# Kernel tuning notes

Measured on AMD Instinct MI355X. Metric: run time of the kernel, lower is better.

## Reference

```python
import jax, jax.numpy as jnp
import numpy as np

N_NODES = 102400
N_EDGES = 1638400
DIMS = [128, 64, 32, 1]  # decoder_dim=128, decoder_l=3, last layer -> 1


def setup_inputs() -> dict:
    key = jax.random.key(0)
    ks = jax.random.split(key, 10)
    inp = {
        'b_z': jax.random.normal(ks[0], (N_NODES, DIMS[0]), jnp.float32),
        'src': jax.random.randint(ks[1], (N_EDGES,), 0, N_NODES, jnp.int64 if jax.config.jax_enable_x64 else jnp.int32),
        'dst': jax.random.randint(ks[2], (N_EDGES,), 0, N_NODES, jnp.int64 if jax.config.jax_enable_x64 else jnp.int32),
        'edge_weight': jax.random.uniform(ks[3], (N_EDGES,), jnp.float32),
        'b_size': 100,
    }
    # GraphConv weights: W [in, out], bias [out] (DGL xavier init; randn ok for ref)
    for i in range(3):
        inp[f'W{i}'] = jax.random.normal(ks[4 + i], (DIMS[i], DIMS[i + 1]), jnp.float32) * (1.0 / np.sqrt(DIMS[i]))
        inp[f'b{i}'] = jnp.zeros((DIMS[i + 1],), jnp.float32)
    return inp


def _gcn_layer(h, src, dst, ew, W, b, activate):
    n = h.shape[0]
    ones = jnp.ones((src.shape[0],), h.dtype)
    # norm='both': symmetric degree normalization with plain (unweighted) degrees
    out_deg = jnp.clip(jax.ops.segment_sum(ones, src, num_segments=n), 1.0)
    in_deg = jnp.clip(jax.ops.segment_sum(ones, dst, num_segments=n), 1.0)
    h = h * (out_deg ** -0.5)[:, None]
    h = h @ W  # in_feats > out_feats: transform before aggregation (DGL order)
    msg = h[src] * ew[:, None]           # [E, out] edge-weighted gather
    agg = jax.ops.segment_sum(msg, dst, num_segments=n)  # scatter-add
    agg = agg * (in_deg ** -0.5)[:, None] + b
    return jnp.tanh(agg) if activate else agg


def reference(b_z, src, dst, edge_weight, b_size, W0, b0, W1, b1, W2, b2):
    h = b_z
    h = _gcn_layer(h, src, dst, edge_weight, W0, b0, True)
    h = _gcn_layer(h, src, dst, edge_weight, W1, b1, True)
    h = _gcn_layer(h, src, dst, edge_weight, W2, b2, False)
    return h.reshape(b_size, -1)
```

## Files before the change

kernel.cpp:

```cpp
#include <hip/hip_runtime.h>
#include <hip/hip_fp16.h>
#include <math.h>

#define N_NODES 102400
#define N_EDGES 1638400
#define NB 100
#define PB 256
#define EPB (N_EDGES/PB)

union H4 { int2 i2; __half h[4]; };

__global__ __launch_bounds__(256) void histA_kernel(const int* __restrict__ src, const int* __restrict__ dst,
                                                    int* __restrict__ histD, int* __restrict__ histS) {
    __shared__ int hD[NB], hS[NB];
    int tid = threadIdx.x;
    if (tid < NB) { hD[tid] = 0; hS[tid] = 0; }
    __syncthreads();
    int base = blockIdx.x * EPB;
    for (int i = tid; i < EPB; i += 256) {
        atomicAdd(&hD[dst[base + i] >> 10], 1);
        atomicAdd(&hS[src[base + i] >> 10], 1);
    }
    __syncthreads();
    if (tid < NB) {
        histD[blockIdx.x * NB + tid] = hD[tid];
        histS[blockIdx.x * NB + tid] = hS[tid];
    }
}

__global__ __launch_bounds__(256) void scanB_kernel(const int* __restrict__ histD, const int* __restrict__ histS,
                                                    int* __restrict__ offD, int* __restrict__ offS,
                                                    int* __restrict__ coarseD, int* __restrict__ coarseS) {
    __shared__ int totD[NB], totS[NB], baseD[NB + 1], baseS[NB + 1];
    int t = threadIdx.x;
    if (t < NB) { int s = 0; for (int k = 0; k < PB; k++) s += histD[k * NB + t]; totD[t] = s; }
    else if (t >= 128 && t < 128 + NB) { int j = t - 128; int s = 0; for (int k = 0; k < PB; k++) s += histS[k * NB + j]; totS[j] = s; }
    __syncthreads();
    if (t == 0)   { int r = 0; for (int j = 0; j < NB; j++) { baseD[j] = r; r += totD[j]; } baseD[NB] = r; }
    if (t == 128) { int r = 0; for (int j = 0; j < NB; j++) { baseS[j] = r; r += totS[j]; } baseS[NB] = r; }
    __syncthreads();
    if (t < NB) { int r = baseD[t]; for (int k = 0; k < PB; k++) { offD[k * NB + t] = r; r += histD[k * NB + t]; } }
    else if (t >= 128 && t < 128 + NB) { int j = t - 128; int r = baseS[j]; for (int k = 0; k < PB; k++) { offS[k * NB + j] = r; r += histS[k * NB + j]; } }
    if (t <= NB) coarseD[t] = baseD[t];
    if (t >= 128 && t <= 128 + NB) coarseS[t - 128] = baseS[t - 128];
}

__global__ __launch_bounds__(256) void partC_kernel(const int* __restrict__ src, const int* __restrict__ dst,
                                                    const float* __restrict__ ew,
                                                    const int* __restrict__ offD, const int* __restrict__ offS,
                                                    int2* __restrict__ partD, int* __restrict__ partS) {
    __shared__ int cD[NB], cS[NB];
    int tid = threadIdx.x;
    if (tid < NB) { cD[tid] = offD[blockIdx.x * NB + tid]; cS[tid] = offS[blockIdx.x * NB + tid]; }
    __syncthreads();
    int base = blockIdx.x * EPB;
    for (int i = tid; i < EPB; i += 256) {
        int s = src[base + i], d = dst[base + i];
        float w = ew[base + i];
        int p = atomicAdd(&cD[d >> 10], 1);
        partD[p] = make_int2(s | ((d & 1023) << 17), __float_as_int(w));
        int q = atomicAdd(&cS[s >> 10], 1);
        partS[q] = s & 1023;
    }
}

__global__ __launch_bounds__(1024) void fineS_kernel(const int* __restrict__ partS, const int* __restrict__ coarseS,
                                                     float* __restrict__ outdeg_inv) {
    __shared__ int hist[1024];
    int tid = threadIdx.x;
    hist[tid] = 0;
    __syncthreads();
    int beg = coarseS[blockIdx.x], end = coarseS[blockIdx.x + 1];
    for (int i = beg + tid; i < end; i += 1024) atomicAdd(&hist[partS[i]], 1);
    __syncthreads();
    outdeg_inv[blockIdx.x * 1024 + tid] = 1.0f / sqrtf((float)max(hist[tid], 1));
}

__global__ __launch_bounds__(1024) void fineD_kernel(const int2* __restrict__ partD, const int* __restrict__ coarseD,
                                                     const float* __restrict__ outdeg_inv,
                                                     int2* __restrict__ edge_perm, int* __restrict__ row_off,
                                                     float* __restrict__ indeg_inv) {
    __shared__ int hist[1024], cursor[1024];
    __shared__ int wsum[16];
    int tid = threadIdx.x, lane = tid & 63, wid = tid >> 6;
    hist[tid] = 0;
    __syncthreads();
    int beg = coarseD[blockIdx.x], end = coarseD[blockIdx.x + 1];
    for (int i = beg + tid; i < end; i += 1024) atomicAdd(&hist[(partD[i].x >> 17) & 1023], 1);
    __syncthreads();
    int v = hist[tid];
    int x = v;
    #pragma unroll
    for (int s = 1; s < 64; s <<= 1) { int t = __shfl_up(x, s, 64); if (lane >= s) x += t; }
    if (lane == 63) wsum[wid] = x;
    __syncthreads();
    if (wid == 0) {
        int ws = (lane < 16) ? wsum[lane] : 0;
        int y = ws;
        #pragma unroll
        for (int s = 1; s < 16; s <<= 1) { int t = __shfl_up(y, s, 64); if (lane >= s) y += t; }
        if (lane < 16) wsum[lane] = y - ws;
    }
    __syncthreads();
    int ex = wsum[wid] + x - v;
    cursor[tid] = beg + ex;
    int node = blockIdx.x * 1024 + tid;
    row_off[node] = beg + ex;
    indeg_inv[node] = 1.0f / sqrtf((float)max(v, 1));
    if (blockIdx.x == NB - 1 && tid == 0) row_off[N_NODES] = N_EDGES;
    __syncthreads();
    for (int i = beg + tid; i < end; i += 1024) {
        int2 t2 = partD[i];
        int d = (t2.x >> 17) & 1023, s = t2.x & 0x1FFFF;
        int p = atomicAdd(&cursor[d], 1);
        float w = __int_as_float(t2.y) * outdeg_inv[s];
        edge_perm[p] = make_int2(s, __float_as_int(w));
    }
}

template<int K, int C, int RN>
__global__ __launch_bounds__(256) void gemm_tile_kernel(
    const float* __restrict__ h, const float* __restrict__ W, __half* __restrict__ out) {
    constexpr int BM = 64;
    constexpr int RM = 4;
    constexpr int KC = 64;
    constexpr int TX = C / RN;
    constexpr int TY = BM / RM;
    static_assert(TX * TY == 256, "bad tile");
    static_assert(RN == 4, "fp16 epilogue assumes RN==4");

    __shared__ float Ws[K * C];
    __shared__ float Hs[KC][BM + 4];

    const int tid = threadIdx.x;
    const long brow = (long)blockIdx.x * BM;

    for (int i = tid; i < K * C; i += 256) Ws[i] = W[i];

    const int tx = tid % TX;
    const int ty = tid / TX;
    float acc[RM][RN] = {};

    const int lr = tid % 16;
    const int lk = tid / 16;

    for (int kc = 0; kc < K; kc += KC) {
        __syncthreads();
        #pragma unroll
        for (int p0 = 0; p0 < BM; p0 += 16) {
            const int r = p0 + lr;
            const float4 hv = *(const float4*)(h + (brow + r) * K + kc + lk * 4);
            Hs[lk * 4 + 0][r] = hv.x;
            Hs[lk * 4 + 1][r] = hv.y;
            Hs[lk * 4 + 2][r] = hv.z;
            Hs[lk * 4 + 3][r] = hv.w;
        }
        __syncthreads();

        #pragma unroll
        for (int k = 0; k < KC; ++k) {
            const float4 a4 = *(const float4*)&Hs[k][ty * RM];
            const float av[RM] = {a4.x, a4.y, a4.z, a4.w};
            float b[RN];
            *(float4*)b = *(const float4*)&Ws[(kc + k) * C + tx * RN];
            #pragma unroll
            for (int i = 0; i < RM; ++i)
                #pragma unroll
                for (int j = 0; j < RN; ++j)
                    acc[i][j] += av[i] * b[j];
        }
    }

    #pragma unroll
    for (int i = 0; i < RM; ++i) {
        const long row = brow + ty * RM + i;
        __half2 p01 = __floats2half2_rn(acc[i][0], acc[i][1]);
        __half2 p23 = __floats2half2_rn(acc[i][2], acc[i][3]);
        int2 packed = make_int2(*(int*)&p01, *(int*)&p23);
        *(int2*)(out + row * C + tx * RN) = packed;
    }
}

__global__ __launch_bounds__(256) void agg64_gemm_kernel(
    const __half* __restrict__ ht, const int* __restrict__ row_off,
    const int2* __restrict__ ep, const float* __restrict__ indeg_inv,
    const float* __restrict__ b0, const float* __restrict__ W1,
    __half* __restrict__ ht1, int N) {
    __shared__ float W1s[64 * 32];
    __shared__ float h1s[4][64];
    int tid = threadIdx.x;
    {
        const float4* W1v = (const float4*)W1;
        float4* W1sv = (float4*)W1s;
        W1sv[tid] = W1v[tid];
        W1sv[tid + 256] = W1v[tid + 256];
    }
    __syncthreads();

    int wave = (blockIdx.x * blockDim.x + tid) >> 6;
    int lane = tid & 63;
    if (wave >= N) return;
    int chunk = lane & 15;
    int eslot = lane >> 4;
    int beg = row_off[wave], end = row_off[wave + 1];
    const char* htb = (const char*)ht;
    unsigned coff = (unsigned)(chunk << 3);

    float4 a0 = {0, 0, 0, 0}, a1 = {0, 0, 0, 0};
    for (int e = beg; e < end; e += 8) {
        int ei0 = e + eslot, ei1 = e + 4 + eslot;
        int2 d0 = ep[min(ei0, end - 1)];
        int2 d1 = ep[min(ei1, end - 1)];
        float w0 = (ei0 < end) ? __int_as_float(d0.y) : 0.0f;
        float w1 = (ei1 < end) ? __int_as_float(d1.y) : 0.0f;
        H4 r0, r1;
        r0.i2 = *(const int2*)(htb + (((unsigned)d0.x << 7) | coff));
        r1.i2 = *(const int2*)(htb + (((unsigned)d1.x << 7) | coff));
        a0.x = fmaf(__half2float(r0.h[0]), w0, a0.x);
        a0.y = fmaf(__half2float(r0.h[1]), w0, a0.y);
        a0.z = fmaf(__half2float(r0.h[2]), w0, a0.z);
        a0.w = fmaf(__half2float(r0.h[3]), w0, a0.w);
        a1.x = fmaf(__half2float(r1.h[0]), w1, a1.x);
        a1.y = fmaf(__half2float(r1.h[1]), w1, a1.y);
        a1.z = fmaf(__half2float(r1.h[2]), w1, a1.z);
        a1.w = fmaf(__half2float(r1.h[3]), w1, a1.w);
    }
    a0.x += a1.x; a0.y += a1.y; a0.z += a1.z; a0.w += a1.w;
    #pragma unroll
    for (int s = 16; s <= 32; s <<= 1) {
        a0.x += __shfl_xor(a0.x, s, 64);
        a0.y += __shfl_xor(a0.y, s, 64);
        a0.z += __shfl_xor(a0.z, s, 64);
        a0.w += __shfl_xor(a0.w, s, 64);
    }
    int wv = tid >> 6;
    if (eslot == 0) {
        float sc = indeg_inv[wave];
        float4 b = *(const float4*)(b0 + chunk * 4);
        float4 v;
        v.x = tanhf(a0.x * sc + b.x);
        v.y = tanhf(a0.y * sc + b.y);
        v.z = tanhf(a0.z * sc + b.z);
        v.w = tanhf(a0.w * sc + b.w);
        *(float4*)&h1s[wv][chunk * 4] = v;
    }
    int c = lane & 31, half = lane >> 5;
    float t = 0.0f;
    #pragma unroll
    for (int j4 = 0; j4 < 8; ++j4) {
        int k = half * 32 + j4 * 4;
        float4 hh = *(const float4*)&h1s[wv][k];
        t += hh.x * W1s[(k + 0) * 32 + c];
        t += hh.y * W1s[(k + 1) * 32 + c];
        t += hh.z * W1s[(k + 2) * 32 + c];
        t += hh.w * W1s[(k + 3) * 32 + c];
    }
    t += __shfl_xor(t, 32, 64);
    if (half == 0) ht1[(long)wave * 32 + c] = __float2half_rn(t);
}

__global__ void agg32_dot_kernel(const __half* __restrict__ ht, const int* __restrict__ row_off,
                                 const int2* __restrict__ ep,
                                 const float* __restrict__ indeg_inv, const float* __restrict__ bias,
                                 const float* __restrict__ W2, float* __restrict__ ht2, int N) {
    int wave = (blockIdx.x * blockDim.x + threadIdx.x) >> 6;
    int lane = threadIdx.x & 63;
    if (wave >= N) return;
    int chunk = lane & 7;
    int eslot = lane >> 3;
    int beg = row_off[wave], end = row_off[wave + 1];
    const char* htb = (const char*)ht;
    unsigned coff = (unsigned)(chunk << 3);
    float4 a0 = {0, 0, 0, 0}, a1 = {0, 0, 0, 0};
    for (int e = beg; e < end; e += 16) {
        int ei0 = e + eslot, ei1 = e + 8 + eslot;
        int2 d0 = ep[min(ei0, end - 1)];
        int2 d1 = ep[min(ei1, end - 1)];
        float w0 = (ei0 < end) ? __int_as_float(d0.y) : 0.0f;
        float w1 = (ei1 < end) ? __int_as_float(d1.y) : 0.0f;
        H4 r0, r1;
        r0.i2 = *(const int2*)(htb + (((unsigned)d0.x << 6) | coff));
        r1.i2 = *(const int2*)(htb + (((unsigned)d1.x << 6) | coff));
        a0.x = fmaf(__half2float(r0.h[0]), w0, a0.x);
        a0.y = fmaf(__half2float(r0.h[1]), w0, a0.y);
        a0.z = fmaf(__half2float(r0.h[2]), w0, a0.z);
        a0.w = fmaf(__half2float(r0.h[3]), w0, a0.w);
        a1.x = fmaf(__half2float(r1.h[0]), w1, a1.x);
        a1.y = fmaf(__half2float(r1.h[1]), w1, a1.y);
        a1.z = fmaf(__half2float(r1.h[2]), w1, a1.z);
        a1.w = fmaf(__half2float(r1.h[3]), w1, a1.w);
    }
    a0.x += a1.x; a0.y += a1.y; a0.z += a1.z; a0.w += a1.w;
    #pragma unroll
    for (int s = 8; s <= 32; s <<= 1) {
        a0.x += __shfl_xor(a0.x, s, 64);
        a0.y += __shfl_xor(a0.y, s, 64);
        a0.z += __shfl_xor(a0.z, s, 64);
        a0.w += __shfl_xor(a0.w, s, 64);
    }
    float sc = indeg_inv[wave];
    float4 b = *(const float4*)(bias + chunk * 4);
    float4 w2 = *(const float4*)(W2 + chunk * 4);
    float t = tanhf(a0.x * sc + b.x) * w2.x
            + tanhf(a0.y * sc + b.y) * w2.y
            + tanhf(a0.z * sc + b.z) * w2.z
            + tanhf(a0.w * sc + b.w) * w2.w;
    t += __shfl_xor(t, 1, 64);
    t += __shfl_xor(t, 2, 64);
    t += __shfl_xor(t, 4, 64);
    if (lane == 0) ht2[wave] = t;
}

__global__ void agg1_kernel(const float* __restrict__ ht2, const int* __restrict__ row_off,
                            const int2* __restrict__ ep,
                            const float* __restrict__ indeg_inv, const float* __restrict__ bias,
                            float* __restrict__ out, int N) {
    int wave = (blockIdx.x * blockDim.x + threadIdx.x) >> 6;
    int lane = threadIdx.x & 63;
    int sub = lane >> 4;
    int slot = lane & 15;
    int node = wave * 4 + sub;
    if (node >= N) return;
    int beg = row_off[node], end = row_off[node + 1];
    float acc = 0.0f;
    for (int e = beg + slot; e < end; e += 16) {
        int2 t = ep[e];
        acc += ht2[t.x] * __int_as_float(t.y);
    }
    #pragma unroll
    for (int s = 1; s <= 8; s <<= 1) acc += __shfl_xor(acc, s, 64);
    if (slot == 0) out[node] = acc * indeg_inv[node] + bias[0];
}

extern "C" void kernel_launch(void* const* d_in, const int* in_sizes, int n_in,
                              void* d_out, int out_size, void* d_ws, size_t ws_size,
                              hipStream_t stream) {
    const float* b_z = (const float*)d_in[0];
    const int*   src = (const int*)d_in[1];
    const int*   dst = (const int*)d_in[2];
    const float* ew  = (const float*)d_in[3];
    const float* W0 = (const float*)d_in[5];
    const float* b0 = (const float*)d_in[6];
    const float* W1 = (const float*)d_in[7];
    const float* b1 = (const float*)d_in[8];
    const float* W2 = (const float*)d_in[9];
    const float* b2 = (const float*)d_in[10];
    float* out = (float*)d_out;

    const int N = N_NODES;
    const int E = N_EDGES;

    char* p = (char*)d_ws;
    int*   row_off    = (int*)p;            p += (size_t)(N + 4) * 4;
    float* outdeg_inv = (float*)p;          p += (size_t)N * 4;
    float* indeg_inv  = (float*)p;          p += (size_t)N * 4;
    int*   histD      = (int*)p;            p += (size_t)PB * NB * 4;
    int*   histS      = (int*)p;            p += (size_t)PB * NB * 4;
    int*   offD       = (int*)p;            p += (size_t)PB * NB * 4;
    int*   offS       = (int*)p;            p += (size_t)PB * NB * 4;
    int*   coarseD    = (int*)p;            p += (size_t)(NB + 4) * 4;
    int*   coarseS    = (int*)p;            p += (size_t)(NB + 4) * 4;
    int2*  edge_perm  = (int2*)p;           p += (size_t)E * 8;
    float* bufA       = (float*)p;          p += (size_t)N * 64 * 4;
    float* bufB       = (float*)p;
    int2*   partD = (int2*)bufA;
    int*    partS = (int*)bufB;
    __half* ht    = (__half*)bufA;
    __half* ht1   = (__half*)bufB;
    float*  ht2   = bufA;

    histA_kernel<<<PB, 256, 0, stream>>>(src, dst, histD, histS);
    scanB_kernel<<<1, 256, 0, stream>>>(histD, histS, offD, offS, coarseD, coarseS);
    partC_kernel<<<PB, 256, 0, stream>>>(src, dst, ew, offD, offS, partD, partS);
    fineS_kernel<<<NB, 1024, 0, stream>>>(partS, coarseS, outdeg_inv);
    fineD_kernel<<<NB, 1024, 0, stream>>>(partD, coarseD, outdeg_inv, edge_perm, row_off, indeg_inv);

    gemm_tile_kernel<128, 64, 4><<<N / 64, 256, 0, stream>>>(b_z, W0, ht);

    agg64_gemm_kernel<<<N / 4, 256, 0, stream>>>(ht, row_off, edge_perm, indeg_inv, b0, W1, ht1, N);

    agg32_dot_kernel<<<N / 4, 256, 0, stream>>>(ht1, row_off, edge_perm, indeg_inv, b1, W2, ht2, N);

    agg1_kernel<<<N / 16, 256, 0, stream>>>(ht2, row_off, edge_perm, indeg_inv, b2, out, N);
}
```

Baseline: 345.4 us.

## Parallelize scan, persist agg64 waves with register-held W1, spread tanh across lanes

The single-block scan now uses 1024 threads, with 8 threads per bucket splitting the 256 partial histograms, which shortens its serial loops. The layer-1 aggregation kernel becomes a grid-stride persistent kernel with 2048 blocks. Each lane keeps its W1 column in registers instead of staging W1 in shared memory on every block. The edge loop is unrolled to 16 edges per iteration and tanh is spread so each lane computes one channel. The layer-2 kernel also spreads tanh across lanes and halves the duplicated reduction. The changes trade more registers per thread and an explicit lgkmcnt wait (no barrier) for fewer redundant tanh calls and lower per-block setup.

```diff
diff --git a/kernel.cpp b/kernel.cpp
--- a/kernel.cpp
+++ b/kernel.cpp
@@ -28,21 +28,53 @@
     }
 }
 
-__global__ __launch_bounds__(256) void scanB_kernel(const int* __restrict__ histD, const int* __restrict__ histS,
-                                                    int* __restrict__ offD, int* __restrict__ offS,
-                                                    int* __restrict__ coarseD, int* __restrict__ coarseS) {
-    __shared__ int totD[NB], totS[NB], baseD[NB + 1], baseS[NB + 1];
-    int t = threadIdx.x;
-    if (t < NB) { int s = 0; for (int k = 0; k < PB; k++) s += histD[k * NB + t]; totD[t] = s; }
-    else if (t >= 128 && t < 128 + NB) { int j = t - 128; int s = 0; for (int k = 0; k < PB; k++) s += histS[k * NB + j]; totS[j] = s; }
-    __syncthreads();
-    if (t == 0)   { int r = 0; for (int j = 0; j < NB; j++) { baseD[j] = r; r += totD[j]; } baseD[NB] = r; }
-    if (t == 128) { int r = 0; for (int j = 0; j < NB; j++) { baseS[j] = r; r += totS[j]; } baseS[NB] = r; }
-    __syncthreads();
-    if (t < NB) { int r = baseD[t]; for (int k = 0; k < PB; k++) { offD[k * NB + t] = r; r += histD[k * NB + t]; } }
-    else if (t >= 128 && t < 128 + NB) { int j = t - 128; int r = baseS[j]; for (int k = 0; k < PB; k++) { offS[k * NB + j] = r; r += histS[k * NB + j]; } }
-    if (t <= NB) coarseD[t] = baseD[t];
-    if (t >= 128 && t <= 128 + NB) coarseS[t - 128] = baseS[t - 128];
+__global__ __launch_bounds__(1024) void scanB_kernel(const int* __restrict__ histD, const int* __restrict__ histS,
+                                                     int* __restrict__ offD, int* __restrict__ offS,
+                                                     int* __restrict__ coarseD, int* __restrict__ coarseS) {
+    __shared__ int pD[NB][8], pS[NB][8];
+    __shared__ int baseD[NB + 1], baseS[NB + 1];
+    int tid = threadIdx.x;
+    int j = tid >> 3, s = tid & 7;
+    if (j < NB) {
+        int sd = 0, ss = 0;
+        for (int k = s * 32; k < s * 32 + 32; ++k) {
+            sd += histD[k * NB + j];
+            ss += histS[k * NB + j];
+        }
+        pD[j][s] = sd; pS[j][s] = ss;
+    }
+    __syncthreads();
+    if (tid == 0) {
+        int r = 0;
+        for (int q = 0; q < NB; ++q) {
+            int t = 0;
+            #pragma unroll
+            for (int s2 = 0; s2 < 8; ++s2) t += pD[q][s2];
+            baseD[q] = r; r += t;
+        }
+        baseD[NB] = r;
+    }
+    if (tid == 512) {
+        int r = 0;
+        for (int q = 0; q < NB; ++q) {
+            int t = 0;
+            #pragma unroll
+            for (int s2 = 0; s2 < 8; ++s2) t += pS[q][s2];
+            baseS[q] = r; r += t;
+        }
+        baseS[NB] = r;
+    }
+    __syncthreads();
+    if (j < NB) {
+        int r = baseD[j];
+        for (int s2 = 0; s2 < s; ++s2) r += pD[j][s2];
+        for (int k = s * 32; k < s * 32 + 32; ++k) { offD[k * NB + j] = r; r += histD[k * NB + j]; }
+        int r2 = baseS[j];
+        for (int s2 = 0; s2 < s; ++s2) r2 += pS[j][s2];
+        for (int k = s * 32; k < s * 32 + 32; ++k) { offS[k * NB + j] = r2; r2 += histS[k * NB + j]; }
+    }
+    if (tid <= NB) coarseD[tid] = baseD[tid];
+    if (tid >= 512 && tid <= 512 + NB) coarseS[tid - 512] = baseS[tid - 512];
 }
 
 __global__ __launch_bounds__(256) void partC_kernel(const int* __restrict__ src, const int* __restrict__ dst,
@@ -186,77 +218,89 @@
     const int2* __restrict__ ep, const float* __restrict__ indeg_inv,
     const float* __restrict__ b0, const float* __restrict__ W1,
     __half* __restrict__ ht1, int N) {
-    __shared__ float W1s[64 * 32];
     __shared__ float h1s[4][64];
-    int tid = threadIdx.x;
-    {
-        const float4* W1v = (const float4*)W1;
-        float4* W1sv = (float4*)W1s;
-        W1sv[tid] = W1v[tid];
-        W1sv[tid + 256] = W1v[tid + 256];
-    }
-    __syncthreads();
-
-    int wave = (blockIdx.x * blockDim.x + tid) >> 6;
-    int lane = tid & 63;
-    if (wave >= N) return;
-    int chunk = lane & 15;
-    int eslot = lane >> 4;
-    int beg = row_off[wave], end = row_off[wave + 1];
+    const int tid = threadIdx.x;
+    const int lane = tid & 63;
+    const int wv = tid >> 6;
+    const int chunk = lane & 15;
+    const int eslot = lane >> 4;
+    const int hf = lane >> 5;
+    const int c = lane & 31;
+
+    float w1reg[32];
+    #pragma unroll
+    for (int j = 0; j < 32; ++j) w1reg[j] = W1[(hf * 32 + j) * 32 + c];
+    const float bch = b0[(chunk << 2) | eslot];
     const char* htb = (const char*)ht;
-    unsigned coff = (unsigned)(chunk << 3);
-
-    float4 a0 = {0, 0, 0, 0}, a1 = {0, 0, 0, 0};
-    for (int e = beg; e < end; e += 8) {
-        int ei0 = e + eslot, ei1 = e + 4 + eslot;
-        int2 d0 = ep[min(ei0, end - 1)];
-        int2 d1 = ep[min(ei1, end - 1)];
-        float w0 = (ei0 < end) ? __int_as_float(d0.y) : 0.0f;
-        float w1 = (ei1 < end) ? __int_as_float(d1.y) : 0.0f;
-        H4 r0, r1;
-        r0.i2 = *(const int2*)(htb + (((unsigned)d0.x << 7) | coff));
-        r1.i2 = *(const int2*)(htb + (((unsigned)d1.x << 7) | coff));
-        a0.x = fmaf(__half2float(r0.h[0]), w0, a0.x);
-        a0.y = fmaf(__half2float(r0.h[1]), w0, a0.y);
-        a0.z = fmaf(__half2float(r0.h[2]), w0, a0.z);
-        a0.w = fmaf(__half2float(r0.h[3]), w0, a0.w);
-        a1.x = fmaf(__half2float(r1.h[0]), w1, a1.x);
-        a1.y = fmaf(__half2float(r1.h[1]), w1, a1.y);
-        a1.z = fmaf(__half2float(r1.h[2]), w1, a1.z);
-        a1.w = fmaf(__half2float(r1.h[3]), w1, a1.w);
-    }
-    a0.x += a1.x; a0.y += a1.y; a0.z += a1.z; a0.w += a1.w;
-    #pragma unroll
-    for (int s = 16; s <= 32; s <<= 1) {
-        a0.x += __shfl_xor(a0.x, s, 64);
-        a0.y += __shfl_xor(a0.y, s, 64);
-        a0.z += __shfl_xor(a0.z, s, 64);
-        a0.w += __shfl_xor(a0.w, s, 64);
-    }
-    int wv = tid >> 6;
-    if (eslot == 0) {
-        float sc = indeg_inv[wave];
-        float4 b = *(const float4*)(b0 + chunk * 4);
-        float4 v;
-        v.x = tanhf(a0.x * sc + b.x);
-        v.y = tanhf(a0.y * sc + b.y);
-        v.z = tanhf(a0.z * sc + b.z);
-        v.w = tanhf(a0.w * sc + b.w);
-        *(float4*)&h1s[wv][chunk * 4] = v;
-    }
-    int c = lane & 31, half = lane >> 5;
-    float t = 0.0f;
-    #pragma unroll
-    for (int j4 = 0; j4 < 8; ++j4) {
-        int k = half * 32 + j4 * 4;
-        float4 hh = *(const float4*)&h1s[wv][k];
-        t += hh.x * W1s[(k + 0) * 32 + c];
-        t += hh.y * W1s[(k + 1) * 32 + c];
-        t += hh.z * W1s[(k + 2) * 32 + c];
-        t += hh.w * W1s[(k + 3) * 32 + c];
-    }
-    t += __shfl_xor(t, 32, 64);
-    if (half == 0) ht1[(long)wave * 32 + c] = __float2half_rn(t);
+    const unsigned coff = (unsigned)(chunk << 3);
+
+    const int wave0 = (blockIdx.x * blockDim.x + tid) >> 6;
+    const int nwaves = (gridDim.x * blockDim.x) >> 6;
+
+    for (int node = wave0; node < N; node += nwaves) {
+        const int beg = row_off[node], end = row_off[node + 1];
+        const int em1 = end - 1;
+        float4 a0 = {0, 0, 0, 0}, a1 = {0, 0, 0, 0}, a2 = {0, 0, 0, 0}, a3 = {0, 0, 0, 0};
+        for (int e = beg; e < end; e += 16) {
+            const int ei0 = e + eslot, ei1 = ei0 + 4, ei2 = ei0 + 8, ei3 = ei0 + 12;
+            int2 d0 = ep[min(ei0, em1)];
+            int2 d1 = ep[min(ei1, em1)];
+            int2 d2 = ep[min(ei2, em1)];
+            int2 d3 = ep[min(ei3, em1)];
+            float w0 = (ei0 < end) ? __int_as_float(d0.y) : 0.0f;
+            float w1 = (ei1 < end) ? __int_as_float(d1.y) : 0.0f;
+            float w2 = (ei2 < end) ? __int_as_float(d2.y) : 0.0f;
+            float w3 = (ei3 < end) ? __int_as_float(d3.y) : 0.0f;
+            H4 r0, r1, r2, r3;
+            r0.i2 = *(const int2*)(htb + (((unsigned)d0.x << 7) | coff));
+            r1.i2 = *(const int2*)(htb + (((unsigned)d1.x << 7) | coff));
+            r2.i2 = *(const int2*)(htb + (((unsigned)d2.x << 7) | coff));
+            r3.i2 = *(const int2*)(htb + (((unsigned)d3.x << 7) | coff));
+            a0.x = fmaf(__half2float(r0.h[0]), w0, a0.x);
+            a0.y = fmaf(__half2float(r0.h[1]), w0, a0.y);
+            a0.z = fmaf(__half2float(r0.h[2]), w0, a0.z);
+            a0.w = fmaf(__half2float(r0.h[3]), w0, a0.w);
+            a1.x = fmaf(__half2float(r1.h[0]), w1, a1.x);
+            a1.y = fmaf(__half2float(r1.h[1]), w1, a1.y);
+            a1.z = fmaf(__half2float(r1.h[2]), w1, a1.z);
+            a1.w = fmaf(__half2float(r1.h[3]), w1, a1.w);
+            a2.x = fmaf(__half2float(r2.h[0]), w2, a2.x);
+            a2.y = fmaf(__half2float(r2.h[1]), w2, a2.y);
+            a2.z = fmaf(__half2float(r2.h[2]), w2, a2.z);
+            a2.w = fmaf(__half2float(r2.h[3]), w2, a2.w);
+            a3.x = fmaf(__half2float(r3.h[0]), w3, a3.x);
+            a3.y = fmaf(__half2float(r3.h[1]), w3, a3.y);
+            a3.z = fmaf(__half2float(r3.h[2]), w3, a3.z);
+            a3.w = fmaf(__half2float(r3.h[3]), w3, a3.w);
+        }
+        a0.x += a1.x + a2.x + a3.x;
+        a0.y += a1.y + a2.y + a3.y;
+        a0.z += a1.z + a2.z + a3.z;
+        a0.w += a1.w + a2.w + a3.w;
+        #pragma unroll
+        for (int s = 16; s <= 32; s <<= 1) {
+            a0.x += __shfl_xor(a0.x, s, 64);
+            a0.y += __shfl_xor(a0.y, s, 64);
+            a0.z += __shfl_xor(a0.z, s, 64);
+            a0.w += __shfl_xor(a0.w, s, 64);
+        }
+        const float sc = indeg_inv[node];
+        float vsel = (eslot == 0) ? a0.x : (eslot == 1) ? a0.y : (eslot == 2) ? a0.z : a0.w;
+        vsel = tanhf(fmaf(vsel, sc, bch));
+        h1s[wv][(chunk << 2) | eslot] = vsel;
+        asm volatile("s_waitcnt lgkmcnt(0)" ::: "memory");
+        float t = 0.0f;
+        #pragma unroll
+        for (int j4 = 0; j4 < 8; ++j4) {
+            const float4 hh = *(const float4*)&h1s[wv][hf * 32 + j4 * 4];
+            t = fmaf(hh.x, w1reg[j4 * 4 + 0], t);
+            t = fmaf(hh.y, w1reg[j4 * 4 + 1], t);
+            t = fmaf(hh.z, w1reg[j4 * 4 + 2], t);
+            t = fmaf(hh.w, w1reg[j4 * 4 + 3], t);
+        }
+        t += __shfl_xor(t, 32, 64);
+        if (hf == 0) ht1[(long)node * 32 + c] = __float2half_rn(t);
+    }
 }
 
 __global__ void agg32_dot_kernel(const __half* __restrict__ ht, const int* __restrict__ row_off,
@@ -298,17 +342,14 @@
         a0.z += __shfl_xor(a0.z, s, 64);
         a0.w += __shfl_xor(a0.w, s, 64);
     }
+    int q = eslot & 3;
+    int ch = (chunk << 2) | q;
     float sc = indeg_inv[wave];
-    float4 b = *(const float4*)(bias + chunk * 4);
-    float4 w2 = *(const float4*)(W2 + chunk * 4);
-    float t = tanhf(a0.x * sc + b.x) * w2.x
-            + tanhf(a0.y * sc + b.y) * w2.y
-            + tanhf(a0.z * sc + b.z) * w2.z
-            + tanhf(a0.w * sc + b.w) * w2.w;
-    t += __shfl_xor(t, 1, 64);
-    t += __shfl_xor(t, 2, 64);
-    t += __shfl_xor(t, 4, 64);
-    if (lane == 0) ht2[wave] = t;
+    float vsel = (q == 0) ? a0.x : (q == 1) ? a0.y : (q == 2) ? a0.z : a0.w;
+    float t = tanhf(fmaf(vsel, sc, bias[ch])) * W2[ch];
+    #pragma unroll
+    for (int s = 1; s <= 32; s <<= 1) t += __shfl_xor(t, s, 64);
+    if (lane == 0) ht2[wave] = 0.5f * t;
 }
 
 __global__ void agg1_kernel(const float* __restrict__ ht2, const int* __restrict__ row_off,
@@ -370,14 +411,14 @@
     float*  ht2   = bufA;
 
     histA_kernel<<<PB, 256, 0, stream>>>(src, dst, histD, histS);
-    scanB_kernel<<<1, 256, 0, stream>>>(histD, histS, offD, offS, coarseD, coarseS);
+    scanB_kernel<<<1, 1024, 0, stream>>>(histD, histS, offD, offS, coarseD, coarseS);
     partC_kernel<<<PB, 256, 0, stream>>>(src, dst, ew, offD, offS, partD, partS);
     fineS_kernel<<<NB, 1024, 0, stream>>>(partS, coarseS, outdeg_inv);
     fineD_kernel<<<NB, 1024, 0, stream>>>(partD, coarseD, outdeg_inv, edge_perm, row_off, indeg_inv);
 
     gemm_tile_kernel<128, 64, 4><<<N / 64, 256, 0, stream>>>(b_z, W0, ht);
 
-    agg64_gemm_kernel<<<N / 4, 256, 0, stream>>>(ht, row_off, edge_perm, indeg_inv, b0, W1, ht1, N);
+    agg64_gemm_kernel<<<2048, 256, 0, stream>>>(ht, row_off, edge_perm, indeg_inv, b0, W1, ht1, N);
 
     agg32_dot_kernel<<<N / 4, 256, 0, stream>>>(ht1, row_off, edge_perm, indeg_inv, b1, W2, ht2, N);
 
```

Result: slower. 369.7 us (+7.0%).
